# Kernel tuning notes

Hardware: AMD Instinct MI355X
Metric: run time of the kernel (lower is better)

The kernel has to match this reference:

```python
import jax, jax.numpy as jnp
import numpy as np

N_IN = 1048576   # coords at feat_depth (fine level)
N_OUT = 524288   # coords at feat_depth + 1 (pooled level)
E = 4194304      # neighbour pairs from hash_tree.get_neighbours
C = 64           # feature channels
NT = 3           # ntypes columns


def setup_inputs() -> dict:
    key = jax.random.key(0)
    k1, k2, k3, k4 = jax.random.split(key, 4)
    feat = jax.random.normal(k1, (N_IN, C), dtype=jnp.float32)
    src_ids = jax.random.randint(k2, (E,), 0, N_OUT, dtype=jnp.int32)
    tgt_ids = jax.random.randint(k3, (E,), 0, N_IN, dtype=jnp.int32)
    # ntypes may contain -1 for missing neighbours; rows with any -1 are masked out
    ntypes = jax.random.randint(k4, (E, NT), -1, 8, dtype=jnp.int32)
    return {"feat": feat, "src_ids": src_ids, "tgt_ids": tgt_ids,
            "ntypes": ntypes, "dim_size": N_OUT, "feat_depth": 2}


def reference(feat, src_ids, tgt_ids, ntypes, dim_size, feat_depth):
    # p_masks = torch.all(ntypes >= 0, dim=1)
    p_masks = jnp.all(ntypes >= 0, axis=1)                      # [E]
    # route masked edges into a drop bucket at index dim_size
    seg = jnp.where(p_masks, src_ids, dim_size)                 # [E]
    gathered = feat[tgt_ids]                                    # [E, C]
    out = jax.ops.segment_max(gathered, seg,
                              num_segments=dim_size + 1)[:dim_size]  # [N_out, C]
    # torch_scatter.scatter_max leaves untouched rows at the init fill; emulate
    # by zeroing empty segments (which segment_max leaves at -inf)
    out = jnp.where(jnp.isneginf(out), jnp.float32(0.0), out)
    return (out, feat_depth + 1)
```

## Files before the change

### kernel.cpp

```cpp
#include <hip/hip_runtime.h>
#include <math.h>

#define CCH 64
#define NLIST 64
#define BIN_CHUNK 4096
#define BIN_EPT 16
#define WROWS 128
#define WSHIFT 7
#define NB2 64
#define CAP2 1280
#define SPILL_CAP 131072

typedef float f4v __attribute__((ext_vector_type(4)));

__device__ __forceinline__ void nt_store_f4(float4 v, float4* p) {
    f4v x; x.x = v.x; x.y = v.y; x.z = v.z; x.w = v.w;
    __builtin_nontemporal_store(x, (f4v*)p);
}

__device__ __forceinline__ void atomicMaxF(float* addr, float v) {
    if (v >= 0.0f) atomicMax((int*)addr, __float_as_int(v));
    else           atomicMin((unsigned int*)addr, __float_as_uint(v));
}


__global__ __launch_bounds__(256) void fill_neginf_kernel(float4* out, int n4) {
    int i = blockIdx.x * blockDim.x + threadIdx.x;
    int stride = gridDim.x * blockDim.x;
    const float4 v = make_float4(-INFINITY, -INFINITY, -INFINITY, -INFINITY);
    for (; i < n4; i += stride) out[i] = v;
}

__global__ __launch_bounds__(256) void scatter_max_kernel(
        const float4* __restrict__ feat4, const int* __restrict__ src,
        const int* __restrict__ tgt, const int* __restrict__ ntypes,
        float* __restrict__ out, int E) {
    int gid = blockIdx.x * blockDim.x + threadIdx.x;
    int e = gid >> 4, q = gid & 15;
    if (e >= E) return;
    int n0 = ntypes[e*3+0], n1 = ntypes[e*3+1], n2 = ntypes[e*3+2];
    if ((n0 | n1 | n2) < 0) return;
    float4 f = feat4[(size_t)tgt[e] * 16 + q];
    float* o = out + (size_t)src[e] * CCH + q * 4;
    atomicMaxF(o+0, f.x); atomicMaxF(o+1, f.y);
    atomicMaxF(o+2, f.z); atomicMaxF(o+3, f.w);
}

__global__ __launch_bounds__(256) void finalize_kernel(
        float4* out, int n4, const int* feat_depth, float* scalar_slot) {
    int i = blockIdx.x * blockDim.x + threadIdx.x;
    int stride = gridDim.x * blockDim.x;
    for (; i < n4; i += stride) {
        float4 v = out[i];
        v.x = (v.x == -INFINITY) ? 0.0f : v.x;
        v.y = (v.y == -INFINITY) ? 0.0f : v.y;
        v.z = (v.z == -INFINITY) ? 0.0f : v.z;
        v.w = (v.w == -INFINITY) ? 0.0f : v.w;
        out[i] = v;
    }
    if (blockIdx.x == 0 && threadIdx.x == 0)
        scalar_slot[0] = (float)(feat_depth[0] + 1);
}


__global__ __launch_bounds__(256) void zero4_kernel(int4* p, long long n4) {
    long long i = blockIdx.x * (long long)blockDim.x + threadIdx.x;
    long long stride = gridDim.x * (long long)blockDim.x;
    const int4 z = make_int4(0, 0, 0, 0);
    for (; i < n4; i += stride) p[i] = z;
}

__global__ __launch_bounds__(256) void bin_kernel(
        const int* __restrict__ src, const int* __restrict__ tgt,
        const int* __restrict__ ntypes,
        unsigned long long* __restrict__ lists, int listCap,
        int* __restrict__ gcur,
        unsigned long long* __restrict__ spill, int spillCap,
        int* __restrict__ spillCur,
        int shift, int E, int numChunks) {
    __shared__ unsigned long long pairs[BIN_CHUNK];
    __shared__ int hist[NLIST];
    __shared__ int lstart[NLIST];
    __shared__ int offs[NLIST];
    __shared__ int gbase[NLIST];
    __shared__ int sh_tot;

    for (int chunk = blockIdx.x; chunk < numChunks; chunk += gridDim.x) {
        long long e0 = (long long)chunk * BIN_CHUNK + (long long)threadIdx.x * BIN_EPT;

        if (threadIdx.x < NLIST) hist[threadIdx.x] = 0;
        __syncthreads();

        unsigned long long myPack[BIN_EPT];
        int myP[BIN_EPT];

        #pragma unroll
        for (int g = 0; g < BIN_EPT / 4; ++g) {
            long long eg = e0 + g * 4;
            int4 s4, t4, n0, n1, n2;
            if (eg + 4 <= E) {
                s4 = *(const int4*)(src + eg);
                t4 = *(const int4*)(tgt + eg);
                const int4* np = (const int4*)(ntypes + eg * 3);
                n0 = np[0]; n1 = np[1]; n2 = np[2];
            } else {
                s4 = make_int4(0,0,0,0); t4 = s4;
                n0 = make_int4(-1,-1,-1,-1); n1 = n0; n2 = n0;
                for (int k = 0; k < 4; ++k) {
                    long long e = eg + k;
                    if (e < E) {
                        (&s4.x)[k] = src[e]; (&t4.x)[k] = tgt[e];
                        int a = ntypes[e*3], b = ntypes[e*3+1], c = ntypes[e*3+2];
                        (&n0.x)[k] = a | b | c;
                        (&n1.x)[k] = 0; (&n2.x)[k] = 0;
                        continue;
                    }
                }
                int ntm[4] = {n0.x, n0.y, n0.z, n0.w};
                for (int k = 0; k < 4; ++k) {
                    int i = g*4 + k;
                    bool ok = (eg + k < E) && (ntm[k] >= 0);
                    int r = (&s4.x)[k];
                    myP[i] = ok ? (r >> shift) : -1;
                    myPack[i] = ((unsigned long long)(unsigned)r << 32) |
                                (unsigned)(&t4.x)[k];
                    if (ok) atomicAdd(&hist[myP[i]], 1);
                }
                continue;
            }
            int m0 = n0.x | n0.y | n0.z;
            int m1 = n0.w | n1.x | n1.y;
            int m2 = n1.z | n1.w | n2.x;
            int m3 = n2.y | n2.z | n2.w;
            int mm[4] = {m0, m1, m2, m3};
            int rr[4] = {s4.x, s4.y, s4.z, s4.w};
            int tt[4] = {t4.x, t4.y, t4.z, t4.w};
            #pragma unroll
            for (int k = 0; k < 4; ++k) {
                int i = g*4 + k;
                bool ok = mm[k] >= 0;
                myP[i] = ok ? (rr[k] >> shift) : -1;
                myPack[i] = ((unsigned long long)(unsigned)rr[k] << 32) |
                            (unsigned)tt[k];
                if (ok) atomicAdd(&hist[myP[i]], 1);
            }
        }
        __syncthreads();

        if (threadIdx.x < NLIST) {
            int h = hist[threadIdx.x];
            int incl = h;
            for (int o = 1; o < NLIST; o <<= 1) {
                int x = __shfl_up(incl, o, NLIST);
                if ((int)threadIdx.x >= o) incl += x;
            }
            lstart[threadIdx.x] = incl - h;
            offs[threadIdx.x]   = incl - h;
            if (threadIdx.x == NLIST - 1) sh_tot = incl;
            gbase[threadIdx.x] = atomicAdd(&gcur[threadIdx.x], h);
        }
        __syncthreads();

        #pragma unroll
        for (int i = 0; i < BIN_EPT; ++i) {
            int p = myP[i];
            if (p >= 0) {
                int pos = atomicAdd(&offs[p], 1);
                pairs[pos] = myPack[i];
            }
        }
        __syncthreads();

        int tot = sh_tot;
        for (int i = threadIdx.x; i < tot; i += 256) {
            unsigned long long pk = pairs[i];
            int p = (int)(pk >> 32) >> shift;
            int gpos = gbase[p] + (i - lstart[p]);
            if (gpos < listCap) {
                lists[(size_t)p * listCap + gpos] = pk;
            } else {
                int sp = atomicAdd(spillCur, 1);
                if (sp < spillCap) spill[sp] = pk;
            }
        }
        __syncthreads();
    }
}

__global__ __launch_bounds__(256) void bin2_kernel(
        const unsigned long long* __restrict__ lists, int listCap,
        const int* __restrict__ gcur,
        unsigned long long* __restrict__ sub, int* __restrict__ cur2,
        unsigned long long* __restrict__ spill, int spillCap,
        int* __restrict__ spillCur, int wpl) {
    __shared__ unsigned long long pr[BIN_CHUNK];
    __shared__ int hist[NB2], lstart[NB2], offs[NB2], gbase[NB2];
    __shared__ int sh_tot;
    int l = blockIdx.x & (NLIST - 1);
    int s = blockIdx.x >> 6;
    int cnt = gcur[l]; if (cnt > listCap) cnt = listCap;
    const unsigned long long* lst = lists + (size_t)l * listCap;
    int wmask = wpl - 1;

    for (int start = s * BIN_CHUNK; start < cnt; start += 16 * BIN_CHUNK) {
        int n = cnt - start; if (n > BIN_CHUNK) n = BIN_CHUNK;
        if (threadIdx.x < NB2) hist[threadIdx.x] = 0;
        __syncthreads();

        unsigned long long my[BIN_EPT]; int myw[BIN_EPT];
        #pragma unroll
        for (int k = 0; k < BIN_EPT; ++k) {
            int i = k * 256 + threadIdx.x;
            if (i < n) {
                unsigned long long pk = lst[start + i];
                int w = ((int)(pk >> 32) >> WSHIFT) & wmask;
                my[k] = pk; myw[k] = w;
                atomicAdd(&hist[w], 1);
            } else myw[k] = -1;
        }
        __syncthreads();

        if (threadIdx.x == 0) {
            int run = 0;
            for (int w = 0; w < wpl; ++w) {
                lstart[w] = run; offs[w] = run; run += hist[w];
            }
            sh_tot = run;
        }
        __syncthreads();
        if ((int)threadIdx.x < wpl)
            gbase[threadIdx.x] =
                atomicAdd(&cur2[l * wpl + threadIdx.x], hist[threadIdx.x]);
        __syncthreads();

        #pragma unroll
        for (int k = 0; k < BIN_EPT; ++k) {
            if (myw[k] >= 0) {
                int pos = atomicAdd(&offs[myw[k]], 1);
                pr[pos] = my[k];
            }
        }
        __syncthreads();

        int tot = sh_tot;
        for (int i = threadIdx.x; i < tot; i += 256) {
            unsigned long long pk = pr[i];
            int w = ((int)(pk >> 32) >> WSHIFT) & wmask;
            int gpos = gbase[w] + (i - lstart[w]);
            if (gpos < CAP2) {
                sub[((size_t)(l * wpl + w)) * CAP2 + gpos] = pk;
            } else {
                int sp = atomicAdd(spillCur, 1);
                if (sp < spillCap) spill[sp] = pk;
            }
        }
        __syncthreads();
    }
}

__global__ __launch_bounds__(512, 8) void fused_kernel(
        const float* __restrict__ feat,
        const unsigned long long* __restrict__ sub,
        const int* __restrict__ cur2,
        float4* __restrict__ out4,
        const int* __restrict__ feat_depth, float* __restrict__ scalar_slot) {
    __shared__ unsigned int tile[WROWS * CCH];
    __shared__ unsigned long long stage[8][64];
    int w = blockIdx.x;
    if (w == 0 && threadIdx.x == 0)
        scalar_slot[0] = (float)(feat_depth[0] + 1);

    for (int i = threadIdx.x; i < WROWS * CCH; i += 512) tile[i] = 0u;
    __syncthreads();

    int cnt = cur2[w]; if (cnt > CAP2) cnt = CAP2;
    const unsigned long long* sl = sub + (size_t)w * CAP2;
    int lane = threadIdx.x & 63;
    int wid = threadIdx.x >> 6;

    for (int i0 = wid * 64; i0 < cnt; i0 += 8 * 64) {
        int m = cnt - i0; if (m > 64) m = 64;
        if (lane < m) stage[wid][lane] = sl[i0 + lane];
        int j = 0;
        for (; j + 8 <= m; j += 8) {
            unsigned long long pk[8];
            #pragma unroll
            for (int u = 0; u < 8; ++u) pk[u] = stage[wid][j + u];
            float f[8]; int rl[8];
            #pragma unroll
            for (int u = 0; u < 8; ++u) {
                int t = (int)(pk[u] & 0xffffffffu);
                rl[u] = ((int)(pk[u] >> 32)) & (WROWS - 1);
                f[u] = feat[(size_t)t * CCH + lane];
            }
            #pragma unroll
            for (int u = 0; u < 8; ++u) {
                unsigned int b = __float_as_uint(f[u]);
                unsigned int key = b ^ ((unsigned int)((int)b >> 31) | 0x80000000u);
                atomicMax(&tile[rl[u] * CCH + lane], key);
            }
        }
        for (; j < m; ++j) {
            unsigned long long pk = stage[wid][j];
            int t = (int)(pk & 0xffffffffu);
            int rl = ((int)(pk >> 32)) & (WROWS - 1);
            unsigned int b = __float_as_uint(feat[(size_t)t * CCH + lane]);
            unsigned int key = b ^ ((unsigned int)((int)b >> 31) | 0x80000000u);
            atomicMax(&tile[rl * CCH + lane], key);
        }
    }
    __syncthreads();

    const uint4* t4 = (const uint4*)tile;
    for (int i = threadIdx.x; i < WROWS * CCH / 4; i += 512) {
        uint4 k = t4[i];
        float4 v;
        v.x = (k.x == 0u) ? 0.0f
              : __uint_as_float((k.x & 0x80000000u) ? (k.x ^ 0x80000000u) : ~k.x);
        v.y = (k.y == 0u) ? 0.0f
              : __uint_as_float((k.y & 0x80000000u) ? (k.y ^ 0x80000000u) : ~k.y);
        v.z = (k.z == 0u) ? 0.0f
              : __uint_as_float((k.z & 0x80000000u) ? (k.z ^ 0x80000000u) : ~k.z);
        v.w = (k.w == 0u) ? 0.0f
              : __uint_as_float((k.w & 0x80000000u) ? (k.w ^ 0x80000000u) : ~k.w);
        nt_store_f4(v, out4 + (size_t)w * (WROWS * (CCH / 4)) + i);
    }
}

__global__ __launch_bounds__(256) void spill_kernel(
        const float4* __restrict__ feat4,
        const unsigned long long* __restrict__ spill,
        const int* __restrict__ spillCur, int spillCap,
        float* __restrict__ out) {
    int n = *spillCur; if (n > spillCap) n = spillCap;
    long long total = (long long)n * 16;
    long long stride = (long long)gridDim.x * blockDim.x;
    for (long long i = blockIdx.x * (long long)blockDim.x + threadIdx.x;
         i < total; i += stride) {
        int e = (int)(i >> 4), q = (int)(i & 15);
        unsigned long long pk = spill[e];
        int r = (int)(pk >> 32);
        int t = (int)(pk & 0xffffffffu);
        float4 f = feat4[(size_t)t * 16 + q];
        float* o = out + (size_t)r * CCH + q * 4;
        atomicMaxF(o+0, f.x); atomicMaxF(o+1, f.y);
        atomicMaxF(o+2, f.z); atomicMaxF(o+3, f.w);
    }
}

__global__ __launch_bounds__(256) void repair_kernel(
        const float4* __restrict__ feat4, const int* __restrict__ src,
        const int* __restrict__ tgt, const int* __restrict__ ntypes,
        const int* __restrict__ spillCur, int spillCap,
        float* __restrict__ out, int E) {
    if (*spillCur <= spillCap) return;
    long long total = (long long)E * 16;
    long long stride = (long long)gridDim.x * blockDim.x;
    for (long long i = blockIdx.x * (long long)blockDim.x + threadIdx.x;
         i < total; i += stride) {
        int e = (int)(i >> 4), q = (int)(i & 15);
        if ((ntypes[e*3] | ntypes[e*3+1] | ntypes[e*3+2]) < 0) continue;
        float4 f = feat4[(size_t)tgt[e] * 16 + q];
        float* o = out + (size_t)src[e] * CCH + q * 4;
        atomicMaxF(o+0, f.x); atomicMaxF(o+1, f.y);
        atomicMaxF(o+2, f.z); atomicMaxF(o+3, f.w);
    }
}

extern "C" void kernel_launch(void* const* d_in, const int* in_sizes, int n_in,
                              void* d_out, int out_size, void* d_ws, size_t ws_size,
                              hipStream_t stream) {
    const float* feat       = (const float*)d_in[0];
    const int*   src_ids    = (const int*)d_in[1];
    const int*   tgt_ids    = (const int*)d_in[2];
    const int*   ntypes     = (const int*)d_in[3];
    const int*   feat_depth = (const int*)d_in[5];
    float* out = (float*)d_out;

    const int E = in_sizes[1];
    const int nout_elems = out_size - 1;
    const int N = nout_elems / CCH;
    const int n4 = nout_elems / 4;

    int shift1 = 0;
    while (((long long)(N - 1) >> shift1) > (NLIST - 1)) ++shift1;
    int wpl = (shift1 >= WSHIFT) ? (1 << (shift1 - WSHIFT)) : 0;
    int windows = (wpl > 0) ? ((N + WROWS - 1) >> WSHIFT) : 0;

    size_t wsInts = ws_size / sizeof(int);
    size_t zeroInts = (size_t)NLIST + windows + 16;
    int LC1 = 0;
    if (wpl >= 1 && wpl <= NB2 && windows > 0 && (N % WROWS) == 0 &&
        (zeroInts % 4) == 0) {
        for (int lc = 69632; lc >= 49152; lc -= 10240) {
            size_t need = zeroInts + 2ull * SPILL_CAP +
                          2ull * NLIST * lc + 2ull * windows * CAP2;
            if (need <= wsInts) { LC1 = lc; break; }
        }
    }

    if (LC1 == 0) {
        fill_neginf_kernel<<<2048, 256, 0, stream>>>((float4*)out, n4);
        long long total = (long long)E * 16;
        int blocks = (int)((total + 255) / 256);
        scatter_max_kernel<<<blocks, 256, 0, stream>>>(
            (const float4*)feat, src_ids, tgt_ids, ntypes, out, E);
        finalize_kernel<<<2048, 256, 0, stream>>>(
            (float4*)out, n4, feat_depth, out + nout_elems);
        return;
    }

    int* gcur     = (int*)d_ws;
    int* cur2     = gcur + NLIST;
    int* spillCur = cur2 + windows;
    unsigned long long* spill  = (unsigned long long*)(spillCur + 16);
    unsigned long long* lists1 = spill + SPILL_CAP;
    unsigned long long* sub    = lists1 + (size_t)NLIST * LC1;

    zero4_kernel<<<16, 256, 0, stream>>>((int4*)d_ws, (long long)(zeroInts / 4));

    int numChunks = (E + BIN_CHUNK - 1) / BIN_CHUNK;
    int binGrid = numChunks < 4096 ? numChunks : 4096;
    bin_kernel<<<binGrid, 256, 0, stream>>>(
        src_ids, tgt_ids, ntypes, lists1, LC1, gcur,
        spill, SPILL_CAP, spillCur, shift1, E, numChunks);

    bin2_kernel<<<NLIST * 16, 256, 0, stream>>>(
        lists1, LC1, gcur, sub, cur2, spill, SPILL_CAP, spillCur, wpl);

    fused_kernel<<<windows, 512, 0, stream>>>(
        feat, sub, cur2, (float4*)out, feat_depth, out + nout_elems);

    spill_kernel<<<2048, 256, 0, stream>>>(
        (const float4*)feat, spill, spillCur, SPILL_CAP, out);
    repair_kernel<<<4096, 256, 0, stream>>>(
        (const float4*)feat, src_ids, tgt_ids, ntypes,
        spillCur, SPILL_CAP, out, E);
}
```

Measured before the change: 205.6 us.

## Pack binned edge pairs into 32-bit words and double first-level lists

Binned (src,tgt) pairs are now stored as 32-bit words holding the target index plus the local row bits within a list, instead of 64-bit pairs. This halves the bytes written and read by bin, bin2 and the fused gather kernel. The first-level bin count goes from 64 to 128 so that the local row bits plus target bits fit in 32 bits. The shuffle scan is replaced by a serial single-thread prefix loop, list capacities shrink, and spilled entries are rebuilt into full 64-bit pairs, which adds a little serial work per chunk.

```diff
diff --git a/kernel.cpp b/kernel.cpp
--- a/kernel.cpp
+++ b/kernel.cpp
@@ -2,7 +2,7 @@
 #include <math.h>
 
 #define CCH 64
-#define NLIST 64
+#define NLIST 128
 #define BIN_CHUNK 4096
 #define BIN_EPT 16
 #define WROWS 128
@@ -73,17 +73,18 @@
 __global__ __launch_bounds__(256) void bin_kernel(
         const int* __restrict__ src, const int* __restrict__ tgt,
         const int* __restrict__ ntypes,
-        unsigned long long* __restrict__ lists, int listCap,
+        unsigned int* __restrict__ lists, int listCap,
         int* __restrict__ gcur,
         unsigned long long* __restrict__ spill, int spillCap,
         int* __restrict__ spillCur,
-        int shift, int E, int numChunks) {
+        int shift, int tbits, int E, int numChunks) {
     __shared__ unsigned long long pairs[BIN_CHUNK];
     __shared__ int hist[NLIST];
     __shared__ int lstart[NLIST];
     __shared__ int offs[NLIST];
     __shared__ int gbase[NLIST];
     __shared__ int sh_tot;
+    const unsigned lmask = (1u << shift) - 1u;
 
     for (int chunk = blockIdx.x; chunk < numChunks; chunk += gridDim.x) {
         long long e0 = (long long)chunk * BIN_CHUNK + (long long)threadIdx.x * BIN_EPT;
@@ -147,18 +148,16 @@
         }
         __syncthreads();
 
-        if (threadIdx.x < NLIST) {
-            int h = hist[threadIdx.x];
-            int incl = h;
-            for (int o = 1; o < NLIST; o <<= 1) {
-                int x = __shfl_up(incl, o, NLIST);
-                if ((int)threadIdx.x >= o) incl += x;
-            }
-            lstart[threadIdx.x] = incl - h;
-            offs[threadIdx.x]   = incl - h;
-            if (threadIdx.x == NLIST - 1) sh_tot = incl;
-            gbase[threadIdx.x] = atomicAdd(&gcur[threadIdx.x], h);
-        }
+        if (threadIdx.x == 0) {
+            int run = 0;
+            for (int p = 0; p < NLIST; ++p) {
+                lstart[p] = run; offs[p] = run; run += hist[p];
+            }
+            sh_tot = run;
+        }
+        __syncthreads();
+        if (threadIdx.x < NLIST)
+            gbase[threadIdx.x] = atomicAdd(&gcur[threadIdx.x], hist[threadIdx.x]);
         __syncthreads();
 
         #pragma unroll
@@ -174,10 +173,12 @@
         int tot = sh_tot;
         for (int i = threadIdx.x; i < tot; i += 256) {
             unsigned long long pk = pairs[i];
-            int p = (int)(pk >> 32) >> shift;
+            unsigned r = (unsigned)(pk >> 32);
+            unsigned t = (unsigned)(pk & 0xffffffffu);
+            int p = (int)(r >> shift);
             int gpos = gbase[p] + (i - lstart[p]);
             if (gpos < listCap) {
-                lists[(size_t)p * listCap + gpos] = pk;
+                lists[(size_t)p * listCap + gpos] = ((r & lmask) << tbits) | t;
             } else {
                 int sp = atomicAdd(spillCur, 1);
                 if (sp < spillCap) spill[sp] = pk;
@@ -188,32 +189,34 @@
 }
 
 __global__ __launch_bounds__(256) void bin2_kernel(
-        const unsigned long long* __restrict__ lists, int listCap,
+        const unsigned int* __restrict__ lists, int listCap,
         const int* __restrict__ gcur,
-        unsigned long long* __restrict__ sub, int* __restrict__ cur2,
+        unsigned int* __restrict__ sub, int* __restrict__ cur2,
         unsigned long long* __restrict__ spill, int spillCap,
-        int* __restrict__ spillCur, int wpl) {
-    __shared__ unsigned long long pr[BIN_CHUNK];
+        int* __restrict__ spillCur, int wpl, int shift, int tbits) {
+    __shared__ unsigned int pr[BIN_CHUNK];
     __shared__ int hist[NB2], lstart[NB2], offs[NB2], gbase[NB2];
     __shared__ int sh_tot;
     int l = blockIdx.x & (NLIST - 1);
-    int s = blockIdx.x >> 6;
+    int s = blockIdx.x / NLIST;
     int cnt = gcur[l]; if (cnt > listCap) cnt = listCap;
-    const unsigned long long* lst = lists + (size_t)l * listCap;
+    const unsigned int* lst = lists + (size_t)l * listCap;
     int wmask = wpl - 1;
+    int wsh = tbits + WSHIFT;
+    unsigned tmask = (tbits >= 32) ? 0xffffffffu : ((1u << tbits) - 1u);
 
     for (int start = s * BIN_CHUNK; start < cnt; start += 16 * BIN_CHUNK) {
         int n = cnt - start; if (n > BIN_CHUNK) n = BIN_CHUNK;
         if (threadIdx.x < NB2) hist[threadIdx.x] = 0;
         __syncthreads();
 
-        unsigned long long my[BIN_EPT]; int myw[BIN_EPT];
+        unsigned int my[BIN_EPT]; int myw[BIN_EPT];
         #pragma unroll
         for (int k = 0; k < BIN_EPT; ++k) {
             int i = k * 256 + threadIdx.x;
             if (i < n) {
-                unsigned long long pk = lst[start + i];
-                int w = ((int)(pk >> 32) >> WSHIFT) & wmask;
+                unsigned int pk = lst[start + i];
+                int w = (int)(pk >> wsh) & wmask;
                 my[k] = pk; myw[k] = w;
                 atomicAdd(&hist[w], 1);
             } else myw[k] = -1;
@@ -244,14 +247,18 @@
 
         int tot = sh_tot;
         for (int i = threadIdx.x; i < tot; i += 256) {
-            unsigned long long pk = pr[i];
-            int w = ((int)(pk >> 32) >> WSHIFT) & wmask;
+            unsigned int pk = pr[i];
+            int w = (int)(pk >> wsh) & wmask;
             int gpos = gbase[w] + (i - lstart[w]);
             if (gpos < CAP2) {
                 sub[((size_t)(l * wpl + w)) * CAP2 + gpos] = pk;
             } else {
                 int sp = atomicAdd(spillCur, 1);
-                if (sp < spillCap) spill[sp] = pk;
+                if (sp < spillCap) {
+                    unsigned long long rfull =
+                        ((unsigned long long)l << shift) | (pk >> tbits);
+                    spill[sp] = (rfull << 32) | (pk & tmask);
+                }
             }
         }
         __syncthreads();
@@ -260,12 +267,12 @@
 
 __global__ __launch_bounds__(512, 8) void fused_kernel(
         const float* __restrict__ feat,
-        const unsigned long long* __restrict__ sub,
+        const unsigned int* __restrict__ sub,
         const int* __restrict__ cur2,
-        float4* __restrict__ out4,
+        float4* __restrict__ out4, int tbits,
         const int* __restrict__ feat_depth, float* __restrict__ scalar_slot) {
     __shared__ unsigned int tile[WROWS * CCH];
-    __shared__ unsigned long long stage[8][64];
+    __shared__ unsigned int stage[8][64];
     int w = blockIdx.x;
     if (w == 0 && threadIdx.x == 0)
         scalar_slot[0] = (float)(feat_depth[0] + 1);
@@ -274,23 +281,24 @@
     __syncthreads();
 
     int cnt = cur2[w]; if (cnt > CAP2) cnt = CAP2;
-    const unsigned long long* sl = sub + (size_t)w * CAP2;
+    const unsigned int* sl = sub + (size_t)w * CAP2;
     int lane = threadIdx.x & 63;
     int wid = threadIdx.x >> 6;
+    unsigned tmask = (tbits >= 32) ? 0xffffffffu : ((1u << tbits) - 1u);
 
     for (int i0 = wid * 64; i0 < cnt; i0 += 8 * 64) {
         int m = cnt - i0; if (m > 64) m = 64;
         if (lane < m) stage[wid][lane] = sl[i0 + lane];
         int j = 0;
         for (; j + 8 <= m; j += 8) {
-            unsigned long long pk[8];
+            unsigned int pk[8];
             #pragma unroll
             for (int u = 0; u < 8; ++u) pk[u] = stage[wid][j + u];
             float f[8]; int rl[8];
             #pragma unroll
             for (int u = 0; u < 8; ++u) {
-                int t = (int)(pk[u] & 0xffffffffu);
-                rl[u] = ((int)(pk[u] >> 32)) & (WROWS - 1);
+                unsigned t = pk[u] & tmask;
+                rl[u] = (int)(pk[u] >> tbits) & (WROWS - 1);
                 f[u] = feat[(size_t)t * CCH + lane];
             }
             #pragma unroll
@@ -301,9 +309,9 @@
             }
         }
         for (; j < m; ++j) {
-            unsigned long long pk = stage[wid][j];
-            int t = (int)(pk & 0xffffffffu);
-            int rl = ((int)(pk >> 32)) & (WROWS - 1);
+            unsigned int pk = stage[wid][j];
+            unsigned t = pk & tmask;
+            int rl = (int)(pk >> tbits) & (WROWS - 1);
             unsigned int b = __float_as_uint(feat[(size_t)t * CCH + lane]);
             unsigned int key = b ^ ((unsigned int)((int)b >> 31) | 0x80000000u);
             atomicMax(&tile[rl * CCH + lane], key);
@@ -377,13 +385,16 @@
     const int*   feat_depth = (const int*)d_in[5];
     float* out = (float*)d_out;
 
-    const int E = in_sizes[1];
+    const int E    = in_sizes[1];
+    const int N_IN = in_sizes[0] / CCH;
     const int nout_elems = out_size - 1;
     const int N = nout_elems / CCH;
     const int n4 = nout_elems / 4;
 
     int shift1 = 0;
     while (((long long)(N - 1) >> shift1) > (NLIST - 1)) ++shift1;
+    int tbits = 1;
+    while (((long long)(N_IN - 1) >> tbits) != 0) ++tbits;
     int wpl = (shift1 >= WSHIFT) ? (1 << (shift1 - WSHIFT)) : 0;
     int windows = (wpl > 0) ? ((N + WROWS - 1) >> WSHIFT) : 0;
 
@@ -391,10 +402,10 @@
     size_t zeroInts = (size_t)NLIST + windows + 16;
     int LC1 = 0;
     if (wpl >= 1 && wpl <= NB2 && windows > 0 && (N % WROWS) == 0 &&
-        (zeroInts % 4) == 0) {
-        for (int lc = 69632; lc >= 49152; lc -= 10240) {
+        (zeroInts % 4) == 0 && tbits + shift1 <= 32) {
+        for (int lc = 32768; lc >= 24576; lc -= 4096) {
             size_t need = zeroInts + 2ull * SPILL_CAP +
-                          2ull * NLIST * lc + 2ull * windows * CAP2;
+                          (size_t)NLIST * lc + (size_t)windows * CAP2;
             if (need <= wsInts) { LC1 = lc; break; }
         }
     }
@@ -413,23 +424,24 @@
     int* gcur     = (int*)d_ws;
     int* cur2     = gcur + NLIST;
     int* spillCur = cur2 + windows;
-    unsigned long long* spill  = (unsigned long long*)(spillCur + 16);
-    unsigned long long* lists1 = spill + SPILL_CAP;
-    unsigned long long* sub    = lists1 + (size_t)NLIST * LC1;
-
-    zero4_kernel<<<16, 256, 0, stream>>>((int4*)d_ws, (long long)(zeroInts / 4));
+    unsigned long long* spill = (unsigned long long*)(spillCur + 16);
+    unsigned int* lists1 = (unsigned int*)(spill + SPILL_CAP);
+    unsigned int* sub    = lists1 + (size_t)NLIST * LC1;
+
+    zero4_kernel<<<8, 256, 0, stream>>>((int4*)d_ws, (long long)(zeroInts / 4));
 
     int numChunks = (E + BIN_CHUNK - 1) / BIN_CHUNK;
     int binGrid = numChunks < 4096 ? numChunks : 4096;
     bin_kernel<<<binGrid, 256, 0, stream>>>(
         src_ids, tgt_ids, ntypes, lists1, LC1, gcur,
-        spill, SPILL_CAP, spillCur, shift1, E, numChunks);
+        spill, SPILL_CAP, spillCur, shift1, tbits, E, numChunks);
 
     bin2_kernel<<<NLIST * 16, 256, 0, stream>>>(
-        lists1, LC1, gcur, sub, cur2, spill, SPILL_CAP, spillCur, wpl);
+        lists1, LC1, gcur, sub, cur2, spill, SPILL_CAP, spillCur,
+        wpl, shift1, tbits);
 
     fused_kernel<<<windows, 512, 0, stream>>>(
-        feat, sub, cur2, (float4*)out, feat_depth, out + nout_elems);
+        feat, sub, cur2, (float4*)out, tbits, feat_depth, out + nout_elems);
 
     spill_kernel<<<2048, 256, 0, stream>>>(
         (const float4*)feat, spill, spillCur, SPILL_CAP, out);
```

Result: no change. 203.6 us (-1.0%).
